# Performance work log

Hardware: AMD Instinct MI355X
Metric: run time of the kernel (lower is better)

Reference implementation:

```python
import jax, jax.numpy as jnp
import numpy as np

N_NODES = 50000
N_EDGES = 800000
NFEAT = 512
NHID = 128
NCLASS = 40


def setup_inputs() -> dict:
    key = jax.random.key(0)
    ks = jax.random.split(key, 12)
    s = lambda fan_in: 1.0 / np.sqrt(fan_in)
    return {
        "x": jax.random.normal(ks[0], (N_NODES, NFEAT), dtype=jnp.float32),
        "edge_src": jax.random.randint(ks[1], (N_EDGES,), 0, N_NODES, dtype=jnp.int32),
        "edge_dst": jax.random.randint(ks[2], (N_EDGES,), 0, N_NODES, dtype=jnp.int32),
        "edge_val": jax.random.uniform(ks[3], (N_EDGES,), dtype=jnp.float32) * 0.1,
        # GraphConvolution 1: nfeat -> nhid
        "W1": jax.random.uniform(ks[4], (NFEAT, NHID), jnp.float32, -s(NFEAT), s(NFEAT)),
        "b1": jnp.zeros((NHID,), jnp.float32),
        # res1 Linear: nfeat -> nhid (stored as [in, out])
        "Wr1": jax.random.uniform(ks[5], (NFEAT, NHID), jnp.float32, -s(NFEAT), s(NFEAT)),
        "br1": jnp.zeros((NHID,), jnp.float32),
        # GraphConvolution 2: 2*nhid -> nclass
        "W2": jax.random.uniform(ks[6], (2 * NHID, NCLASS), jnp.float32, -s(2 * NHID), s(2 * NHID)),
        "b2": jnp.zeros((NCLASS,), jnp.float32),
        # res2 Linear: 2*nhid -> nclass
        "Wr2": jax.random.uniform(ks[7], (2 * NHID, NCLASS), jnp.float32, -s(2 * NHID), s(2 * NHID)),
        "br2": jnp.zeros((NCLASS,), jnp.float32),
    }


def _spmm(edge_src, edge_dst, edge_val, support):
    # adj @ support with adj in COO form: out[d] += val * support[s]
    msgs = edge_val[:, None] * support[edge_src]  # [E, F] irregular gather
    return jax.ops.segment_sum(msgs, edge_dst, num_segments=N_NODES)


def reference(x, edge_src, edge_dst, edge_val, W1, b1, Wr1, br1, W2, b2, Wr2, br2):
    # gc1(x, adj) = adj @ (x @ W1) + b1
    gc1 = _spmm(edge_src, edge_dst, edge_val, x @ W1) + b1
    h = jnp.concatenate([jax.nn.relu(gc1), x @ Wr1 + br1], axis=1)  # [N, 2*nhid]
    # dropout is identity in eval mode
    gc2 = _spmm(edge_src, edge_dst, edge_val, h @ W2) + b2
    h2 = gc2 + (h @ Wr2 + br2)
    return jax.nn.log_softmax(h2, axis=1)
```

## Files before the change

kernel.cpp:

```cpp
#include <hip/hip_runtime.h>
#include <stdint.h>

#define N_NODES 50000
#define N_EDGES 800000
#define NFEAT 512
#define NHID 128
#define NCLASS 40
#define NBLK 3125
#define NBUCK 196

typedef __attribute__((ext_vector_type(8))) __bf16 bf16x8;
typedef __attribute__((ext_vector_type(4))) float f32x4;
typedef _Float16 h2 __attribute__((ext_vector_type(2)));

__device__ __forceinline__ uint16_t f2b(float f) {
  uint32_t x = __float_as_uint(f);
  uint32_t r = (x + 0x7fffu + ((x >> 16) & 1u)) >> 16;
  return (uint16_t)r;
}

__global__ void k_pre2(const float* __restrict__ x, uint16_t* __restrict__ xb,
                       const float* __restrict__ W1, const float* __restrict__ Wr1,
                       const float* __restrict__ W2, const float* __restrict__ Wr2,
                       uint16_t* __restrict__ WT1, uint16_t* __restrict__ WT2,
                       const int* __restrict__ dst, int* __restrict__ bc) {
  int b = blockIdx.x, t = threadIdx.x;
  if (b < 12500) {
    int i = b * 256 + t;
    const float4* p = (const float4*)x + (size_t)i * 2;
    float4 a = p[0], c = p[1];
    union { uint16_t u[8]; uint4 v; } o;
    o.u[0] = f2b(a.x); o.u[1] = f2b(a.y); o.u[2] = f2b(a.z); o.u[3] = f2b(a.w);
    o.u[4] = f2b(c.x); o.u[5] = f2b(c.y); o.u[6] = f2b(c.z); o.u[7] = f2b(c.w);
    ((uint4*)xb)[i] = o.v;
  } else if (b < 13140) {
    int idx = (b - 12500) * 256 + t;
    if (idx < 131072) {
      int n = idx >> 9, k = idx & 511;
      float v = (n < 128) ? W1[(size_t)k * 128 + n] : Wr1[(size_t)k * 128 + (n - 128)];
      WT1[idx] = f2b(v);
    } else {
      int j = idx - 131072;
      int n = j >> 8, k = j & 255;
      float v = 0.f;
      if (n < 40) v = W2[(size_t)k * 40 + n];
      else if (n < 80) v = Wr2[(size_t)k * 40 + (n - 40)];
      WT2[j] = f2b(v);
    }
  } else {
    __shared__ int hist[NBUCK];
    int eb = b - 13140;
    if (t < NBUCK) hist[t] = 0;
    __syncthreads();
    int d = dst[eb * 256 + t];
    atomicAdd(&hist[d >> 8], 1);
    __syncthreads();
    if (t < NBUCK) bc[eb * NBUCK + t] = hist[t];
  }
}

__global__ void k_p2(const int* __restrict__ bc, int* __restrict__ bc2,
                     int* __restrict__ bucketTotal) {
  __shared__ int part[256];
  int k = blockIdx.x, t = threadIdx.x;
  int vals[13];
  int s = 0;
  int base = t * 13;
#pragma unroll
  for (int i = 0; i < 13; i++) {
    int idx = base + i;
    int v = (idx < NBLK) ? bc[idx * NBUCK + k] : 0;
    vals[i] = v;
    s += v;
  }
  part[t] = s;
  __syncthreads();
  for (int o = 1; o < 256; o <<= 1) {
    int v = (t >= o) ? part[t - o] : 0;
    __syncthreads();
    part[t] += v;
    __syncthreads();
  }
  int run = (t == 0) ? 0 : part[t - 1];
#pragma unroll
  for (int i = 0; i < 13; i++) {
    int idx = base + i;
    if (idx < NBLK) {
      bc2[k * NBLK + idx] = run;
      run += vals[i];
    }
  }
  if (t == 255) bucketTotal[k] = part[255];
}

__global__ void k_p4(const int* __restrict__ src, const int* __restrict__ dst,
                     const float* __restrict__ val, const int* __restrict__ bc2,
                     const int* __restrict__ bucketTotal, int2* __restrict__ esc) {
  __shared__ int sc[256];
  __shared__ int start[NBUCK];
  __shared__ int cur[NBUCK];
  int b = blockIdx.x, t = threadIdx.x;
  sc[t] = (t < NBUCK) ? bucketTotal[t] : 0;
  __syncthreads();
  for (int o = 1; o < 256; o <<= 1) {
    int v = (t >= o) ? sc[t - o] : 0;
    __syncthreads();
    sc[t] += v;
    __syncthreads();
  }
  if (t < NBUCK) {
    start[t] = ((t == 0) ? 0 : sc[t - 1]) + bc2[t * NBLK + b];
    cur[t] = 0;
  }
  __syncthreads();
  int e = b * 256 + t;
  int d = dst[e];
  int k = d >> 8;
  int r = atomicAdd(&cur[k], 1);
  esc[start[k] + r] = make_int2(src[e] | ((d & 255) << 16), __float_as_int(val[e]));
}

__global__ void k_p5(const int2* __restrict__ esc, const int* __restrict__ bucketTotal,
                     int2* __restrict__ es, int* __restrict__ offs) {
  __shared__ int bsc[256];
  __shared__ int hist[256];
  __shared__ int sc[256];
  __shared__ int cur[256];
  int k = blockIdx.x, t = threadIdx.x;
  bsc[t] = (t < NBUCK) ? bucketTotal[t] : 0;
  __syncthreads();
  for (int o = 1; o < 256; o <<= 1) {
    int v = (t >= o) ? bsc[t - o] : 0;
    __syncthreads();
    bsc[t] += v;
    __syncthreads();
  }
  int base = (k == 0) ? 0 : bsc[k - 1];
  int n = bsc[k] - base;
  hist[t] = 0;
  __syncthreads();
  for (int i = t; i < n; i += 256) atomicAdd(&hist[esc[base + i].x >> 16], 1);
  __syncthreads();
  sc[t] = hist[t];
  __syncthreads();
  for (int o = 1; o < 256; o <<= 1) {
    int v = (t >= o) ? sc[t - o] : 0;
    __syncthreads();
    sc[t] += v;
    __syncthreads();
  }
  int excl = (t == 0) ? 0 : sc[t - 1];
  int node = k * 256 + t;
  if (node <= N_NODES) offs[node] = base + excl;
  cur[t] = excl;
  __syncthreads();
  for (int i = t; i < n; i += 256) {
    int2 e = esc[base + i];
    int l = e.x >> 16;
    int r = atomicAdd(&cur[l], 1);
    es[base + r] = make_int2(e.x & 0xFFFF, e.y);
  }
}

__global__ __launch_bounds__(256, 2) void k_gemm1(
    const uint16_t* __restrict__ A, const uint16_t* __restrict__ BT, int M,
    _Float16* __restrict__ S1h, uint16_t* __restrict__ h, const float* __restrict__ br1) {
  __shared__ uint16_t Al[128 * 64];
  __shared__ uint16_t Bl[128 * 64];
  const int tid = threadIdx.x;
  const int w = tid >> 6, lane = tid & 63;
  const int wm = w >> 1, wn = w & 1;
  const int m0 = blockIdx.x * 128;
  const int n0 = blockIdx.y * 128;
  const int K = NFEAT;

  f32x4 acc[4][4];
#pragma unroll
  for (int t = 0; t < 4; t++)
#pragma unroll
    for (int u = 0; u < 4; u++) acc[t][u] = (f32x4)0.f;

  const int lrow = lane >> 3;
  const int lcol = lane & 7;

  for (int kb = 0; kb < K / 64; ++kb) {
    __syncthreads();
    const int k0 = kb * 64;
#pragma unroll
    for (int i = 0; i < 4; i++) {
      int rr = (w * 4 + i) * 8 + lrow;
      int ra = m0 + rr;
      if (ra >= M) ra = M - 1;
      const uint16_t* gA = A + (size_t)ra * K + k0 + lcol * 8;
      __builtin_amdgcn_global_load_lds(
          (const __attribute__((address_space(1))) void*)gA,
          (__attribute__((address_space(3))) void*)&Al[(w * 4 + i) * 512], 16, 0, 0);
      int rb = n0 + rr;
      const uint16_t* gB = BT + (size_t)rb * K + k0 + lcol * 8;
      __builtin_amdgcn_global_load_lds(
          (const __attribute__((address_space(1))) void*)gB,
          (__attribute__((address_space(3))) void*)&Bl[(w * 4 + i) * 512], 16, 0, 0);
    }
    __syncthreads();
#pragma unroll
    for (int s = 0; s < 2; s++) {
      bf16x8 av[4], bv[4];
#pragma unroll
      for (int t = 0; t < 4; t++)
        av[t] = *(const bf16x8*)&Al[(wm * 64 + t * 16 + (lane & 15)) * 64 + s * 32 + (lane >> 4) * 8];
#pragma unroll
      for (int u = 0; u < 4; u++)
        bv[u] = *(const bf16x8*)&Bl[(wn * 64 + u * 16 + (lane & 15)) * 64 + s * 32 + (lane >> 4) * 8];
#pragma unroll
      for (int t = 0; t < 4; t++)
#pragma unroll
        for (int u = 0; u < 4; u++)
          acc[t][u] = __builtin_amdgcn_mfma_f32_16x16x32_bf16(av[t], bv[u], acc[t][u], 0, 0, 0);
    }
  }

  const int cl = lane & 15, rq = lane >> 4;
#pragma unroll
  for (int t = 0; t < 4; t++) {
#pragma unroll
    for (int u = 0; u < 4; u++) {
#pragma unroll
      for (int r = 0; r < 4; r++) {
        int m = m0 + wm * 64 + t * 16 + rq * 4 + r;
        int n = n0 + wn * 64 + u * 16 + cl;
        if (m >= M) continue;
        float v = acc[t][u][r];
        if (n < 128)
          S1h[(size_t)m * 128 + n] = (_Float16)v;
        else
          h[(size_t)m * 256 + n] = f2b(v + br1[n - 128]);
      }
    }
  }
}

__global__ __launch_bounds__(256, 2) void k_gemm2(
    const uint16_t* __restrict__ A, const uint16_t* __restrict__ BT, int M,
    _Float16* __restrict__ S2h, float* __restrict__ oacc,
    const float* __restrict__ b2, const float* __restrict__ br2) {
  __shared__ uint16_t Al[128 * 64];
  __shared__ uint16_t Bl[128 * 64];
  const int tid = threadIdx.x;
  const int w = tid >> 6, lane = tid & 63;
  const int wm = w >> 1, wn = w & 1;
  const int m0 = blockIdx.x * 128;
  const int K = 256;

  f32x4 acc[4][4];
#pragma unroll
  for (int t = 0; t < 4; t++)
#pragma unroll
    for (int u = 0; u < 4; u++) acc[t][u] = (f32x4)0.f;

  const int lrow = lane >> 3;
  const int lcol = lane & 7;

  for (int kb = 0; kb < K / 64; ++kb) {
    __syncthreads();
    const int k0 = kb * 64;
#pragma unroll
    for (int i = 0; i < 4; i++) {
      int rr = (w * 4 + i) * 8 + lrow;
      int ra = m0 + rr;
      if (ra >= M) ra = M - 1;
      const uint16_t* gA = A + (size_t)ra * K + k0 + lcol * 8;
      __builtin_amdgcn_global_load_lds(
          (const __attribute__((address_space(1))) void*)gA,
          (__attribute__((address_space(3))) void*)&Al[(w * 4 + i) * 512], 16, 0, 0);
      const uint16_t* gB = BT + (size_t)rr * K + k0 + lcol * 8;
      __builtin_amdgcn_global_load_lds(
          (const __attribute__((address_space(1))) void*)gB,
          (__attribute__((address_space(3))) void*)&Bl[(w * 4 + i) * 512], 16, 0, 0);
    }
    __syncthreads();
#pragma unroll
    for (int s = 0; s < 2; s++) {
      bf16x8 av[4], bv[4];
#pragma unroll
      for (int t = 0; t < 4; t++)
        av[t] = *(const bf16x8*)&Al[(wm * 64 + t * 16 + (lane & 15)) * 64 + s * 32 + (lane >> 4) * 8];
#pragma unroll
      for (int u = 0; u < 4; u++)
        bv[u] = *(const bf16x8*)&Bl[(wn * 64 + u * 16 + (lane & 15)) * 64 + s * 32 + (lane >> 4) * 8];
#pragma unroll
      for (int t = 0; t < 4; t++)
#pragma unroll
        for (int u = 0; u < 4; u++)
          acc[t][u] = __builtin_amdgcn_mfma_f32_16x16x32_bf16(av[t], bv[u], acc[t][u], 0, 0, 0);
    }
  }

  const int cl = lane & 15, rq = lane >> 4;
#pragma unroll
  for (int t = 0; t < 4; t++) {
#pragma unroll
    for (int u = 0; u < 4; u++) {
#pragma unroll
      for (int r = 0; r < 4; r++) {
        int m = m0 + wm * 64 + t * 16 + rq * 4 + r;
        int n = wn * 64 + u * 16 + cl;
        if (m >= M) continue;
        float v = acc[t][u][r];
        if (n < 40) S2h[(size_t)m * 64 + n] = (_Float16)v;
        else if (n < 64) S2h[(size_t)m * 64 + n] = (_Float16)0.f;
        if (n >= 40 && n < 80) oacc[(size_t)m * 64 + (n - 40)] = v + b2[n - 40] + br2[n - 40];
        else if (n >= 80 && n < 104) oacc[(size_t)m * 64 + (n - 40)] = 0.f;
      }
    }
  }
}

__global__ void k_spmm1_csr(const int* __restrict__ offs, const int2* __restrict__ es,
                            const _Float16* __restrict__ S1h, const float* __restrict__ b1,
                            uint16_t* __restrict__ h) {
  int node = blockIdx.x * 4 + (threadIdx.x >> 6);
  if (node >= N_NODES) return;
  int lane = threadIdx.x & 63;
  int eg = lane >> 4;
  int fg = lane & 15;
  int beg = offs[node], end = offs[node + 1];
  h2 acc[4];
#pragma unroll
  for (int j = 0; j < 4; j++) acc[j] = (h2)(_Float16)0.f;
  for (int p = beg; p < end; p += 8) {
    int pa = p + eg, pb = p + 4 + eg;
    bool oka = pa < end, okb = pb < end;
    int2 ea = es[oka ? pa : beg];
    int2 eb = es[okb ? pb : beg];
    float va = oka ? __int_as_float(ea.y) : 0.f;
    float vb = okb ? __int_as_float(eb.y) : 0.f;
    _Float16 vah = (_Float16)va, vbh = (_Float16)vb;
    h2 vva = {vah, vah}, vvb = {vbh, vbh};
    uint4 ga = *(const uint4*)(S1h + (size_t)ea.x * 128 + fg * 8);
    uint4 gb = *(const uint4*)(S1h + (size_t)eb.x * 128 + fg * 8);
    h2* ha = (h2*)&ga;
    h2* hb = (h2*)&gb;
#pragma unroll
    for (int j = 0; j < 4; j++) {
      acc[j] = vva * ha[j] + acc[j];
      acc[j] = vvb * hb[j] + acc[j];
    }
  }
#pragma unroll
  for (int j = 0; j < 4; j++) {
    int b16 = __shfl_xor(__builtin_bit_cast(int, acc[j]), 16, 64);
    acc[j] = acc[j] + __builtin_bit_cast(h2, b16);
    int b32 = __shfl_xor(__builtin_bit_cast(int, acc[j]), 32, 64);
    acc[j] = acc[j] + __builtin_bit_cast(h2, b32);
  }
  if (eg == 0) {
    const float4* bp = (const float4*)(b1 + fg * 8);
    float4 ba = bp[0], bb = bp[1];
    float r0 = (float)acc[0][0] + ba.x, r1 = (float)acc[0][1] + ba.y;
    float r2 = (float)acc[1][0] + ba.z, r3 = (float)acc[1][1] + ba.w;
    float r4 = (float)acc[2][0] + bb.x, r5 = (float)acc[2][1] + bb.y;
    float r6 = (float)acc[3][0] + bb.z, r7 = (float)acc[3][1] + bb.w;
    union { uint16_t u[8]; uint4 v; } o;
    o.u[0] = f2b(r0 > 0.f ? r0 : 0.f); o.u[1] = f2b(r1 > 0.f ? r1 : 0.f);
    o.u[2] = f2b(r2 > 0.f ? r2 : 0.f); o.u[3] = f2b(r3 > 0.f ? r3 : 0.f);
    o.u[4] = f2b(r4 > 0.f ? r4 : 0.f); o.u[5] = f2b(r5 > 0.f ? r5 : 0.f);
    o.u[6] = f2b(r6 > 0.f ? r6 : 0.f); o.u[7] = f2b(r7 > 0.f ? r7 : 0.f);
    *(uint4*)(h + (size_t)node * 256 + fg * 8) = o.v;
  }
}

__global__ void k_spmm2_lsm(const int* __restrict__ offs, const int2* __restrict__ es,
                            const _Float16* __restrict__ S2h, const float* __restrict__ oacc,
                            float* __restrict__ out) {
  int node = blockIdx.x * 4 + (threadIdx.x >> 6);
  if (node >= N_NODES) return;
  int lane = threadIdx.x & 63;
  int eg = lane >> 3;
  int fg = lane & 7;
  int beg = offs[node], end = offs[node + 1];
  h2 acc[4];
#pragma unroll
  for (int j = 0; j < 4; j++) acc[j] = (h2)(_Float16)0.f;
  for (int p = beg; p < end; p += 16) {
    int pa = p + eg, pb = p + 8 + eg;
    bool oka = pa < end, okb = pb < end;
    int2 ea = es[oka ? pa : beg];
    int2 eb = es[okb ? pb : beg];
    float va = oka ? __int_as_float(ea.y) : 0.f;
    float vb = okb ? __int_as_float(eb.y) : 0.f;
    _Float16 vah = (_Float16)va, vbh = (_Float16)vb;
    h2 vva = {vah, vah}, vvb = {vbh, vbh};
    uint4 ga = *(const uint4*)(S2h + (size_t)ea.x * 64 + fg * 8);
    uint4 gb = *(const uint4*)(S2h + (size_t)eb.x * 64 + fg * 8);
    h2* ha = (h2*)&ga;
    h2* hb = (h2*)&gb;
#pragma unroll
    for (int j = 0; j < 4; j++) {
      acc[j] = vva * ha[j] + acc[j];
      acc[j] = vvb * hb[j] + acc[j];
    }
  }
#pragma unroll
  for (int j = 0; j < 4; j++) {
    int b8 = __shfl_xor(__builtin_bit_cast(int, acc[j]), 8, 64);
    acc[j] = acc[j] + __builtin_bit_cast(h2, b8);
    int b16 = __shfl_xor(__builtin_bit_cast(int, acc[j]), 16, 64);
    acc[j] = acc[j] + __builtin_bit_cast(h2, b16);
    int b32 = __shfl_xor(__builtin_bit_cast(int, acc[j]), 32, 64);
    acc[j] = acc[j] + __builtin_bit_cast(h2, b32);
  }
  const float4* op = (const float4*)(oacc + (size_t)node * 64 + fg * 8);
  float4 o0 = op[0], o1 = op[1];
  float v0 = (float)acc[0][0] + o0.x, v1 = (float)acc[0][1] + o0.y;
  float v2 = (float)acc[1][0] + o0.z, v3 = (float)acc[1][1] + o0.w;
  float v4 = (float)acc[2][0] + o1.x, v5 = (float)acc[2][1] + o1.y;
  float v6 = (float)acc[3][0] + o1.z, v7 = (float)acc[3][1] + o1.w;
  bool valid = fg < 5;
  float m01 = v0 > v1 ? v0 : v1, m23 = v2 > v3 ? v2 : v3;
  float m45 = v4 > v5 ? v4 : v5, m67 = v6 > v7 ? v6 : v7;
  float ml = m01 > m23 ? m01 : m23;
  float mh = m45 > m67 ? m45 : m67;
  float mv = ml > mh ? ml : mh;
  mv = valid ? mv : -1e30f;
#pragma unroll
  for (int o = 1; o <= 4; o <<= 1) {
    float t = __shfl_xor(mv, o, 64);
    mv = mv > t ? mv : t;
  }
  float se = 0.f;
  if (valid)
    se = __expf(v0 - mv) + __expf(v1 - mv) + __expf(v2 - mv) + __expf(v3 - mv) +
         __expf(v4 - mv) + __expf(v5 - mv) + __expf(v6 - mv) + __expf(v7 - mv);
#pragma unroll
  for (int o = 1; o <= 4; o <<= 1) se += __shfl_xor(se, o, 64);
  if (eg == 0 && valid) {
    float ls = mv + __logf(se);
    float4 r0 = make_float4(v0 - ls, v1 - ls, v2 - ls, v3 - ls);
    float4 r1 = make_float4(v4 - ls, v5 - ls, v6 - ls, v7 - ls);
    float4* wp = (float4*)(out + (size_t)node * 40 + fg * 8);
    wp[0] = r0;
    wp[1] = r1;
  }
}

extern "C" void kernel_launch(void* const* d_in, const int* in_sizes, int n_in,
                              void* d_out, int out_size, void* d_ws, size_t ws_size,
                              hipStream_t stream) {
  const float* x = (const float*)d_in[0];
  const int* esrc = (const int*)d_in[1];
  const int* edst = (const int*)d_in[2];
  const float* eval = (const float*)d_in[3];
  const float* W1 = (const float*)d_in[4];
  const float* b1 = (const float*)d_in[5];
  const float* Wr1 = (const float*)d_in[6];
  const float* br1 = (const float*)d_in[7];
  const float* W2 = (const float*)d_in[8];
  const float* b2 = (const float*)d_in[9];
  const float* Wr2 = (const float*)d_in[10];
  const float* br2 = (const float*)d_in[11];
  float* out = (float*)d_out;

  char* ws = (char*)d_ws;
  uint16_t* xb   = (uint16_t*)(ws);
  _Float16* S1h  = (_Float16*)(ws + 51200000);
  uint16_t* h    = (uint16_t*)(ws + 64000000);
  uint16_t* WT1  = (uint16_t*)(ws + 89600000);
  uint16_t* WT2  = (uint16_t*)(ws + 89862144);
  _Float16* S2h  = (_Float16*)(ws + 89927680);
  float*    oacc = (float*)(ws + 96327680);
  int*      offs = (int*)(ws + 109127680);
  int2*     es   = (int2*)(ws + 109327696);
  int2*     esc  = (int2*)(ws + 115727696);
  int*      bc   = (int*)(ws + 122127696);
  int*      bc2  = (int*)(ws + 124577696);
  int*      bucketTotal = (int*)(ws + 127027696);

  k_pre2<<<16265, 256, 0, stream>>>(x, xb, W1, Wr1, W2, Wr2, WT1, WT2, edst, bc);
  k_p2<<<NBUCK, 256, 0, stream>>>(bc, bc2, bucketTotal);
  k_p4<<<NBLK, 256, 0, stream>>>(esrc, edst, eval, bc2, bucketTotal, esc);
  k_p5<<<NBUCK, 256, 0, stream>>>(esc, bucketTotal, es, offs);

  dim3 g1(391, 2);
  k_gemm1<<<g1, 256, 0, stream>>>(xb, WT1, N_NODES, S1h, h, br1);

  k_spmm1_csr<<<(N_NODES + 3) / 4, 256, 0, stream>>>(offs, es, S1h, b1, h);

  k_gemm2<<<391, 256, 0, stream>>>(h, WT2, N_NODES, S2h, oacc, b2, br2);

  k_spmm2_lsm<<<(N_NODES + 3) / 4, 256, 0, stream>>>(offs, es, S2h, oacc, out);
}
```

Baseline: 319.9 us.

## Fuse fp32-to-fp16 conversion of x into first GEMM's A-operand load

Removes the separate pass that converted x to bf16 in workspace; GEMM1 now loads fp32 x directly into registers, packs to fp16 and uses f16 MFMA, with W1 weights pre-transposed to fp16. This eliminates a full write and reread of the converted activation matrix and shrinks workspace. In exchange the A operand bypasses LDS, is read redundantly by warps sharing rows and across the two column blocks, and its load latency is less hidden.

```diff
diff --git a/kernel.cpp b/kernel.cpp
--- a/kernel.cpp
+++ b/kernel.cpp
@@ -12,44 +12,40 @@
 typedef __attribute__((ext_vector_type(8))) __bf16 bf16x8;
 typedef __attribute__((ext_vector_type(4))) float f32x4;
 typedef _Float16 h2 __attribute__((ext_vector_type(2)));
+typedef _Float16 f16x8 __attribute__((ext_vector_type(8)));
 
 __device__ __forceinline__ uint16_t f2b(float f) {
   uint32_t x = __float_as_uint(f);
   uint32_t r = (x + 0x7fffu + ((x >> 16) & 1u)) >> 16;
   return (uint16_t)r;
 }
-
-__global__ void k_pre2(const float* __restrict__ x, uint16_t* __restrict__ xb,
-                       const float* __restrict__ W1, const float* __restrict__ Wr1,
+__device__ __forceinline__ uint16_t f2h_bits(float f) {
+  return __builtin_bit_cast(uint16_t, (_Float16)f);
+}
+__device__ __forceinline__ h2 cvt_pk(float a, float b) {
+  return __builtin_bit_cast(h2, __builtin_amdgcn_cvt_pkrtz(a, b));
+}
+
+__global__ void k_pre3(const float* __restrict__ W1, const float* __restrict__ Wr1,
                        const float* __restrict__ W2, const float* __restrict__ Wr2,
-                       uint16_t* __restrict__ WT1, uint16_t* __restrict__ WT2,
+                       uint16_t* __restrict__ WT1h, uint16_t* __restrict__ WT2,
                        const int* __restrict__ dst, int* __restrict__ bc) {
   int b = blockIdx.x, t = threadIdx.x;
-  if (b < 12500) {
-    int i = b * 256 + t;
-    const float4* p = (const float4*)x + (size_t)i * 2;
-    float4 a = p[0], c = p[1];
-    union { uint16_t u[8]; uint4 v; } o;
-    o.u[0] = f2b(a.x); o.u[1] = f2b(a.y); o.u[2] = f2b(a.z); o.u[3] = f2b(a.w);
-    o.u[4] = f2b(c.x); o.u[5] = f2b(c.y); o.u[6] = f2b(c.z); o.u[7] = f2b(c.w);
-    ((uint4*)xb)[i] = o.v;
-  } else if (b < 13140) {
-    int idx = (b - 12500) * 256 + t;
-    if (idx < 131072) {
-      int n = idx >> 9, k = idx & 511;
-      float v = (n < 128) ? W1[(size_t)k * 128 + n] : Wr1[(size_t)k * 128 + (n - 128)];
-      WT1[idx] = f2b(v);
-    } else {
-      int j = idx - 131072;
-      int n = j >> 8, k = j & 255;
-      float v = 0.f;
-      if (n < 40) v = W2[(size_t)k * 40 + n];
-      else if (n < 80) v = Wr2[(size_t)k * 40 + (n - 40)];
-      WT2[j] = f2b(v);
-    }
+  if (b < 512) {
+    int idx = b * 256 + t;
+    int n = idx >> 9, k = idx & 511;
+    float v = (n < 128) ? W1[(size_t)k * 128 + n] : Wr1[(size_t)k * 128 + (n - 128)];
+    WT1h[idx] = f2h_bits(v);
+  } else if (b < 640) {
+    int j = (b - 512) * 256 + t;
+    int n = j >> 8, k = j & 255;
+    float v = 0.f;
+    if (n < 40) v = W2[(size_t)k * 40 + n];
+    else if (n < 80) v = Wr2[(size_t)k * 40 + (n - 40)];
+    WT2[j] = f2b(v);
   } else {
     __shared__ int hist[NBUCK];
-    int eb = b - 13140;
+    int eb = b - 640;
     if (t < NBUCK) hist[t] = 0;
     __syncthreads();
     int d = dst[eb * 256 + t];
@@ -162,17 +158,16 @@
   }
 }
 
-__global__ __launch_bounds__(256, 2) void k_gemm1(
-    const uint16_t* __restrict__ A, const uint16_t* __restrict__ BT, int M,
+__global__ __launch_bounds__(256, 2) void k_gemm1f(
+    const float* __restrict__ x, const uint16_t* __restrict__ BTh, int M,
     _Float16* __restrict__ S1h, uint16_t* __restrict__ h, const float* __restrict__ br1) {
-  __shared__ uint16_t Al[128 * 64];
   __shared__ uint16_t Bl[128 * 64];
   const int tid = threadIdx.x;
   const int w = tid >> 6, lane = tid & 63;
   const int wm = w >> 1, wn = w & 1;
   const int m0 = blockIdx.x * 128;
   const int n0 = blockIdx.y * 128;
-  const int K = NFEAT;
+  const int quad = lane >> 4;
 
   f32x4 acc[4][4];
 #pragma unroll
@@ -183,39 +178,53 @@
   const int lrow = lane >> 3;
   const int lcol = lane & 7;
 
-  for (int kb = 0; kb < K / 64; ++kb) {
+  const float* ap[4];
+#pragma unroll
+  for (int t = 0; t < 4; t++) {
+    int r = m0 + wm * 64 + t * 16 + (lane & 15);
+    if (r >= M) r = M - 1;
+    ap[t] = x + (size_t)r * NFEAT + quad * 8;
+  }
+
+  for (int kb = 0; kb < 8; ++kb) {
     __syncthreads();
     const int k0 = kb * 64;
 #pragma unroll
     for (int i = 0; i < 4; i++) {
       int rr = (w * 4 + i) * 8 + lrow;
-      int ra = m0 + rr;
-      if (ra >= M) ra = M - 1;
-      const uint16_t* gA = A + (size_t)ra * K + k0 + lcol * 8;
-      __builtin_amdgcn_global_load_lds(
-          (const __attribute__((address_space(1))) void*)gA,
-          (__attribute__((address_space(3))) void*)&Al[(w * 4 + i) * 512], 16, 0, 0);
-      int rb = n0 + rr;
-      const uint16_t* gB = BT + (size_t)rb * K + k0 + lcol * 8;
+      const uint16_t* gB = BTh + (size_t)(n0 + rr) * NFEAT + k0 + lcol * 8;
       __builtin_amdgcn_global_load_lds(
           (const __attribute__((address_space(1))) void*)gB,
           (__attribute__((address_space(3))) void*)&Bl[(w * 4 + i) * 512], 16, 0, 0);
     }
+    f16x8 av[4][2];
+#pragma unroll
+    for (int t = 0; t < 4; t++) {
+#pragma unroll
+      for (int s = 0; s < 2; s++) {
+        const float* p = ap[t] + k0 + s * 32;
+        float4 f0 = *(const float4*)p;
+        float4 f1 = *(const float4*)(p + 4);
+        union { h2 hh[4]; f16x8 v; } u;
+        u.hh[0] = cvt_pk(f0.x, f0.y);
+        u.hh[1] = cvt_pk(f0.z, f0.w);
+        u.hh[2] = cvt_pk(f1.x, f1.y);
+        u.hh[3] = cvt_pk(f1.z, f1.w);
+        av[t][s] = u.v;
+      }
+    }
     __syncthreads();
 #pragma unroll
     for (int s = 0; s < 2; s++) {
-      bf16x8 av[4], bv[4];
+      f16x8 bv[4];
+#pragma unroll
+      for (int u = 0; u < 4; u++)
+        bv[u] = *(const f16x8*)&Bl[(wn * 64 + u * 16 + (lane & 15)) * 64 + s * 32 + quad * 8];
 #pragma unroll
       for (int t = 0; t < 4; t++)
-        av[t] = *(const bf16x8*)&Al[(wm * 64 + t * 16 + (lane & 15)) * 64 + s * 32 + (lane >> 4) * 8];
-#pragma unroll
-      for (int u = 0; u < 4; u++)
-        bv[u] = *(const bf16x8*)&Bl[(wn * 64 + u * 16 + (lane & 15)) * 64 + s * 32 + (lane >> 4) * 8];
-#pragma unroll
-      for (int t = 0; t < 4; t++)
 #pragma unroll
         for (int u = 0; u < 4; u++)
-          acc[t][u] = __builtin_amdgcn_mfma_f32_16x16x32_bf16(av[t], bv[u], acc[t][u], 0, 0, 0);
+          acc[t][u] = __builtin_amdgcn_mfma_f32_16x16x32_f16(av[t][s], bv[u], acc[t][u], 0, 0, 0);
     }
   }
 
@@ -461,27 +470,26 @@
   float* out = (float*)d_out;
 
   char* ws = (char*)d_ws;
-  uint16_t* xb   = (uint16_t*)(ws);
-  _Float16* S1h  = (_Float16*)(ws + 51200000);
-  uint16_t* h    = (uint16_t*)(ws + 64000000);
-  uint16_t* WT1  = (uint16_t*)(ws + 89600000);
-  uint16_t* WT2  = (uint16_t*)(ws + 89862144);
-  _Float16* S2h  = (_Float16*)(ws + 89927680);
-  float*    oacc = (float*)(ws + 96327680);
-  int*      offs = (int*)(ws + 109127680);
-  int2*     es   = (int2*)(ws + 109327696);
-  int2*     esc  = (int2*)(ws + 115727696);
-  int*      bc   = (int*)(ws + 122127696);
-  int*      bc2  = (int*)(ws + 124577696);
-  int*      bucketTotal = (int*)(ws + 127027696);
-
-  k_pre2<<<16265, 256, 0, stream>>>(x, xb, W1, Wr1, W2, Wr2, WT1, WT2, edst, bc);
+  _Float16* S1h  = (_Float16*)(ws);
+  uint16_t* h    = (uint16_t*)(ws + 12800000);
+  uint16_t* WT1h = (uint16_t*)(ws + 38400000);
+  uint16_t* WT2  = (uint16_t*)(ws + 38662144);
+  _Float16* S2h  = (_Float16*)(ws + 38727680);
+  float*    oacc = (float*)(ws + 45127680);
+  int*      offs = (int*)(ws + 57927680);
+  int2*     es   = (int2*)(ws + 58127696);
+  int2*     esc  = (int2*)(ws + 64527696);
+  int*      bc   = (int*)(ws + 70927696);
+  int*      bc2  = (int*)(ws + 73377696);
+  int*      bucketTotal = (int*)(ws + 75827696);
+
+  k_pre3<<<3765, 256, 0, stream>>>(W1, Wr1, W2, Wr2, WT1h, WT2, edst, bc);
   k_p2<<<NBUCK, 256, 0, stream>>>(bc, bc2, bucketTotal);
   k_p4<<<NBLK, 256, 0, stream>>>(esrc, edst, eval, bc2, bucketTotal, esc);
   k_p5<<<NBUCK, 256, 0, stream>>>(esc, bucketTotal, es, offs);
 
   dim3 g1(391, 2);
-  k_gemm1<<<g1, 256, 0, stream>>>(xb, WT1, N_NODES, S1h, h, br1);
+  k_gemm1f<<<g1, 256, 0, stream>>>(x, WT1h, N_NODES, S1h, h, br1);
 
   k_spmm1_csr<<<(N_NODES + 3) / 4, 256, 0, stream>>>(offs, es, S1h, b1, h);
 
```

After: 332.9 us. +4.1%, slower.
